# Performance work log

Measured on AMD Instinct MI355X. Metric: run time of the kernel, lower is better.

Reference implementation:

```python
import jax, jax.numpy as jnp
import numpy as np
from jax import lax
from jax.scipy.special import logsumexp

B, T, N = 256, 512, 128


def setup_inputs() -> dict:
    key = jax.random.key(0)
    k1, k2, k3 = jax.random.split(key, 3)
    emissions = jax.random.normal(k1, (B, T, N), dtype=jnp.float32)
    tag_ids = jax.random.randint(k2, (B, T), 0, N, dtype=jnp.int64)
    mask = jnp.ones((B, T), dtype=jnp.int32)
    # learned transition matrix (glorot-uniform-ish init)
    limit = float(np.sqrt(6.0 / (N + N)))
    trans = jax.random.uniform(k3, (N, N), minval=-limit, maxval=limit, dtype=jnp.float32)
    return {"emissions": emissions, "tag_ids": tag_ids, "mask": mask, "trans": trans}


def _sequence_score(emissions, tag_ids, maskf, trans):
    # unary: emission score of the gold tag at each valid step
    unary = jnp.take_along_axis(emissions, tag_ids[:, :, None], axis=2)[..., 0]  # [B,T]
    unary = jnp.sum(unary * maskf, axis=1)
    # binary: transition score between consecutive gold tags
    binary = trans[tag_ids[:, :-1], tag_ids[:, 1:]] * maskf[:, 1:]  # [B,T-1]
    return unary + jnp.sum(binary, axis=1)


def _log_norm(emissions, maskf, trans):
    # forward algorithm over time via lax.scan; alpha: [B,N]
    alpha0 = emissions[:, 0]
    em = jnp.swapaxes(emissions, 0, 1)[1:]   # [T-1,B,N]
    mk = jnp.swapaxes(maskf, 0, 1)[1:]       # [T-1,B]

    def step(alpha, xs):
        emit_t, m_t = xs
        new = logsumexp(alpha[:, :, None] + trans[None], axis=1) + emit_t
        alpha = jnp.where(m_t[:, None] > 0, new, alpha)
        return alpha, None

    alpha, _ = lax.scan(step, alpha0, (em, mk))
    return logsumexp(alpha, axis=1)  # [B]


def _viterbi_decode(emissions, maskf, trans):
    alpha0 = emissions[:, 0]
    em = jnp.swapaxes(emissions, 0, 1)[1:]
    mk = jnp.swapaxes(maskf, 0, 1)[1:]
    idx = jnp.arange(N, dtype=jnp.int32)[None]

    def fwd(alpha, xs):
        emit_t, m_t = xs
        scores = alpha[:, :, None] + trans[None]        # [B,N,N]
        bp = jnp.argmax(scores, axis=1).astype(jnp.int32)  # [B,N]
        new = jnp.max(scores, axis=1) + emit_t
        valid = m_t[:, None] > 0
        alpha = jnp.where(valid, new, alpha)
        bp = jnp.where(valid, bp, idx)  # carry same tag through padding
        return alpha, bp

    alpha, bps = lax.scan(fwd, alpha0, (em, mk))  # bps: [T-1,B,N]
    last_tag = jnp.argmax(alpha, axis=1).astype(jnp.int32)  # [B]

    def bwd(tag, bp_t):
        new_tag = jnp.take_along_axis(bp_t, tag[:, None], axis=1)[:, 0]
        return new_tag, new_tag

    _, tags_rev = lax.scan(bwd, last_tag, bps[::-1])  # [T-1,B]
    tags = jnp.concatenate([tags_rev[::-1], last_tag[None]], axis=0)  # [T,B]
    return jnp.swapaxes(tags, 0, 1)  # [B,T]


def reference(emissions, tag_ids, mask, trans):
    maskf = mask.astype(emissions.dtype)
    log_likelihood = _sequence_score(emissions, tag_ids, maskf, trans) - _log_norm(emissions, maskf, trans)
    predict = _viterbi_decode(emissions, maskf, trans)
    return (log_likelihood, trans, predict)
```

## Files before the change

kernel.cpp:

```cpp
#include <hip/hip_runtime.h>
#include <cmath>

#define BB 256
#define TT 512
#define NN 128
#define LN2F 0.6931471805599453f

typedef __bf16 bf16x8 __attribute__((ext_vector_type(8)));
typedef float floatx4 __attribute__((ext_vector_type(4)));

__device__ __forceinline__ float wave_max64(float v) {
    #pragma unroll
    for (int off = 32; off; off >>= 1) v = fmaxf(v, __shfl_xor(v, off));
    return v;
}
__device__ __forceinline__ float wave_sum64(float v) {
    #pragma unroll
    for (int off = 32; off; off >>= 1) v += __shfl_xor(v, off);
    return v;
}
__device__ __forceinline__ int wave_argmax128(float v0, float v1, int l) {
    float m = fmaxf(v0, v1);
    float wm = wave_max64(m);
    unsigned long long ball = __ballot(m == wm);
    int lane = __ffsll(ball) - 1;
    int idx = (v0 == wm) ? (2 * l) : (2 * l + 1);
    return __shfl(idx, lane);
}

__device__ __forceinline__ __bf16 to_bf16(float f) {
    unsigned u = __float_as_uint(f);
    unsigned r = (u + 0x7FFFu + ((u >> 16) & 1u)) >> 16;
    union { unsigned short s; __bf16 b; } cv;
    cv.s = (unsigned short)r;
    return cv.b;
}

__device__ __forceinline__ int padidx(int i) { return 36 * (i >> 5) + (i & 31); }

__global__ __launch_bounds__(512, 4) void fwd_kernel(
        const float* __restrict__ em, const int* __restrict__ gtags,
        const int* __restrict__ mask, const float* __restrict__ trans,
        float* __restrict__ out_ll, float* __restrict__ out_trans,
        float* __restrict__ outp) {
    const int bi = blockIdx.x;
    const bool isV = bi < BB;
    const int b = isV ? bi : bi - BB;
    const int tid = threadIdx.x;
    const int w = tid >> 6;
    const int l = tid & 63;
    const int j = (l & 15) + 16 * w;
    const int q = l >> 4;
    const int i0 = 32 * q;

    __shared__ __align__(16) float stA[144], stB[144];
    __shared__ __align__(16) __bf16 sbf[2][NN];
    __shared__ unsigned char bp_lds[TT * NN];
    __shared__ unsigned char tags_lds[TT];
    __shared__ unsigned char map_lds[8 * NN];
    __shared__ int entry_sh[8];
    __shared__ int msk[TT];
    __shared__ float piv[2];
    __shared__ float sfin[NN];
    __shared__ float wsum[8];
    __shared__ float llnorm_sh;
    __shared__ int misc[2];

    msk[tid] = mask[b * TT + tid];

    const float* emb = em + (size_t)b * TT * NN;

    if (isV) {
        float4 c0, c1, c2, c3, c4, c5, c6, c7;
        {
            const float* tc = trans + (size_t)i0 * NN + j;
            #define LDC(cc, u) cc.x = tc[(4*u+0)*NN]; cc.y = tc[(4*u+1)*NN]; \
                               cc.z = tc[(4*u+2)*NN]; cc.w = tc[(4*u+3)*NN];
            LDC(c0, 0) LDC(c1, 1) LDC(c2, 2) LDC(c3, 3)
            LDC(c4, 4) LDC(c5, 5) LDC(c6, 6) LDC(c7, 7)
            #undef LDC
        }
        float st = 0.f;
        {
            float a0 = emb[j];
            st = a0;
            if (l < 16) stA[padidx(j)] = a0;
        }
        float e_next = emb[NN + j];
        __syncthreads();

        const float4* apA = (const float4*)(stA + 36 * q);
        const float4* apB = (const float4*)(stB + 36 * q);

        auto VSTEP = [&](int t, const float4* ap, float* dst) {
            const float e_cur = e_next;
            if (t + 1 < TT) e_next = emb[(size_t)(t + 1) * NN + j];
            const int m = msk[t];
            float4 v0 = ap[0], v1 = ap[1], v2 = ap[2], v3 = ap[3],
                   v4 = ap[4], v5 = ap[5], v6 = ap[6], v7 = ap[7];
            float m0 = -INFINITY, m1 = -INFINITY, m2 = -INFINITY, m3 = -INFINITY;
            int u0 = 0, u1 = 0, u2 = 0, u3 = 0;
            #define CH(vv, cc, u) { \
                float a = vv.x + cc.x; u0 = (a > m0) ? u : u0; m0 = fmaxf(m0, a); \
                float bq = vv.y + cc.y; u1 = (bq > m1) ? u : u1; m1 = fmaxf(m1, bq); \
                float c = vv.z + cc.z; u2 = (c > m2) ? u : u2; m2 = fmaxf(m2, c); \
                float d = vv.w + cc.w; u3 = (d > m3) ? u : u3; m3 = fmaxf(m3, d); }
            CH(v0, c0, 0) CH(v1, c1, 1) CH(v2, c2, 2) CH(v3, c3, 3)
            CH(v4, c4, 4) CH(v5, c5, 5) CH(v6, c6, 6) CH(v7, c7, 7)
            #undef CH
            float bv = m0; int bx = i0 + 4 * u0;
            { int id = i0 + 4*u1 + 1; if (m1 > bv || (m1 == bv && id < bx)) { bv = m1; bx = id; } }
            { int id = i0 + 4*u2 + 2; if (m2 > bv || (m2 == bv && id < bx)) { bv = m2; bx = id; } }
            { int id = i0 + 4*u3 + 3; if (m3 > bv || (m3 == bv && id < bx)) { bv = m3; bx = id; } }
            #pragma unroll
            for (int off = 16; off <= 32; off <<= 1) {
                float ov = __shfl_xor(bv, off);
                int oi = __shfl_xor(bx, off);
                if (ov > bv || (ov == bv && oi < bx)) { bv = ov; bx = oi; }
            }
            if (l < 16) {
                float an; int bp;
                if (m) { an = bv + e_cur; bp = bx; }
                else   { an = st;         bp = j;  }
                st = an;
                dst[padidx(j)] = an;
                bp_lds[t * NN + j] = (unsigned char)bp;
            }
            __syncthreads();
        };

        for (int t = 1; t < TT - 1; t += 2) {
            VSTEP(t, apA, stB);
            VSTEP(t + 1, apB, stA);
        }
        VSTEP(TT - 1, apA, stB);

        if (w == 0) {
            float a0 = stB[padidx(2 * l)], a1 = stB[padidx(2 * l + 1)];
            int tg = wave_argmax128(a0, a1, l);
            if (l == 0) { misc[0] = tg; tags_lds[TT - 1] = (unsigned char)tg; }
        }
        if (tid < 64) out_trans[b * 64 + tid] = trans[b * 64 + tid];
        __syncthreads();
        const int lo = 64 * w + 1;
        const int hi = (w == 7) ? (TT - 1) : (64 * w + 64);
        {
            int tA = 2 * l, tB = 2 * l + 1;
            for (int t = hi; t >= lo; --t) {
                tA = bp_lds[t * NN + tA];
                tB = bp_lds[t * NN + tB];
            }
            map_lds[w * NN + 2 * l]     = (unsigned char)tA;
            map_lds[w * NN + 2 * l + 1] = (unsigned char)tB;
        }
        __syncthreads();
        if (tid == 0) {
            int e = misc[0];
            entry_sh[7] = e;
            for (int c = 7; c >= 1; --c) { e = map_lds[c * NN + e]; entry_sh[c - 1] = e; }
        }
        __syncthreads();
        if (l == 0) {
            int tg = entry_sh[w];
            for (int t = hi; t >= lo; --t) {
                tg = bp_lds[t * NN + tg];
                tags_lds[t - 1] = (unsigned char)tg;
            }
        }
        __syncthreads();
        outp[(size_t)b * TT + tid] = (float)tags_lds[tid];
    } else {
        bf16x8 Bf[4];
        #pragma unroll
        for (int kc = 0; kc < 4; ++kc) {
            #pragma unroll
            for (int jj = 0; jj < 8; ++jj) {
                int row = kc * 32 + q * 8 + jj;
                Bf[kc][jj] = to_bf16(__expf(trans[(size_t)row * NN + j]));
            }
        }
        float ss = __expf(emb[j]);
        int kacc = 0;
        if (l < 16) sbf[0][j] = to_bf16(ss);
        if (tid == 0) piv[0] = ss;
        float e_next = emb[NN + j];
        __syncthreads();

        for (int t = 1; t < TT; ++t) {
            const float e_cur = e_next;
            if (t + 1 < TT) e_next = emb[(size_t)(t + 1) * NN + j];
            const int m = msk[t];
            const int p = (t - 1) & 1, qb = t & 1;
            if (m) {
                const __bf16* sp = sbf[p];
                floatx4 acc = {0.f, 0.f, 0.f, 0.f};
                #pragma unroll
                for (int kc = 0; kc < 4; ++kc) {
                    bf16x8 a = *(const bf16x8*)(sp + kc * 32 + q * 8);
                    acc = __builtin_amdgcn_mfma_f32_16x16x32_bf16(a, Bf[kc], acc, 0, 0, 0);
                }
                float dot = acc[0];
                const float pv = piv[p];
                const int k = (int)(__float_as_uint(pv) >> 23) - 127;
                const float scale = __uint_as_float((unsigned)(127 - k) << 23);
                ss = dot * scale * __expf(e_cur);
                if (tid == 0) kacc += k;
            }
            if (l < 16) sbf[qb][j] = to_bf16(ss);
            if (tid == 0) piv[qb] = ss;
            __syncthreads();
        }

        if (l < 16) sfin[j] = ss;
        if (tid == 0) misc[1] = kacc;
        __syncthreads();
        if (w == 0) {
            float v = sfin[2 * l] + sfin[2 * l + 1];
            v = wave_sum64(v);
            if (l == 0) llnorm_sh = __logf(v) + (float)misc[1] * LN2F;
        }
        float acc = 0.f;
        {
            int tg = gtags[b * TT + tid];
            float mf = (float)msk[tid];
            acc = emb[(size_t)tid * NN + tg] * mf;
            if (tid >= 1) {
                int tp = gtags[b * TT + tid - 1];
                acc += trans[tp * NN + tg] * mf;
            }
        }
        acc = wave_sum64(acc);
        if (l == 0) wsum[w] = acc;
        __syncthreads();
        if (tid == 0) {
            float s = 0.f;
            #pragma unroll
            for (int i = 0; i < 8; ++i) s += wsum[i];
            out_ll[b] = s - llnorm_sh;
        }
    }
}

extern "C" void kernel_launch(void* const* d_in, const int* in_sizes, int n_in,
                              void* d_out, int out_size, void* d_ws, size_t ws_size,
                              hipStream_t stream) {
    const float* em = (const float*)d_in[0];
    const int* gtags = (const int*)d_in[1];
    const int* mask = (const int*)d_in[2];
    const float* trans = (const float*)d_in[3];

    float* out = (float*)d_out;
    float* out_ll = out;
    float* out_trans = out + BB;
    float* out_pred = out + BB + NN * NN;

    hipLaunchKernelGGL(fwd_kernel, dim3(2 * BB), dim3(512), 0, stream,
                       em, gtags, mask, trans, out_ll, out_trans, out_pred);
}
```

Baseline: 521.1 us.

## Move Viterbi backpointers to global workspace and transposed trans into LDS

Adds a Viterbi kernel variant that writes backpointers to a global workspace buffer instead of a 64KB LDS array. The freed LDS holds a padded, transposed copy of the transition matrix, which is read as float4 in place of 32 register-held values. The aim is to cut register pressure and LDS footprint per block. The cost is global memory traffic for backpointers, including dependent global reads during the backtrace. The old kernel remains as a fallback when the workspace is too small.

```diff
diff --git a/kernel.cpp b/kernel.cpp
--- a/kernel.cpp
+++ b/kernel.cpp
@@ -5,6 +5,7 @@
 #define TT 512
 #define NN 128
 #define LN2F 0.6931471805599453f
+#define TLS 132
 
 typedef __bf16 bf16x8 __attribute__((ext_vector_type(8)));
 typedef float floatx4 __attribute__((ext_vector_type(4)));
@@ -38,7 +39,207 @@
 
 __device__ __forceinline__ int padidx(int i) { return 36 * (i >> 5) + (i & 31); }
 
-__global__ __launch_bounds__(512, 4) void fwd_kernel(
+__global__ __launch_bounds__(512, 4) void fwd_kernel_g(
+        const float* __restrict__ em, const int* __restrict__ gtags,
+        const int* __restrict__ mask, const float* __restrict__ trans,
+        unsigned char* __restrict__ bpg_all,
+        float* __restrict__ out_ll, float* __restrict__ out_trans,
+        float* __restrict__ outp) {
+    const int bi = blockIdx.x;
+    const bool isV = bi < BB;
+    const int b = isV ? bi : bi - BB;
+    const int tid = threadIdx.x;
+    const int w = tid >> 6;
+    const int l = tid & 63;
+    const int j = (l & 15) + 16 * w;
+    const int q = l >> 4;
+    const int i0 = 32 * q;
+
+    __shared__ __align__(16) float tl[NN * TLS];
+    __shared__ __align__(16) float stA[144], stB[144];
+    __shared__ __align__(16) __bf16 sbf[2][NN];
+    __shared__ unsigned char tags_lds[TT];
+    __shared__ unsigned char map_lds[8 * NN];
+    __shared__ int entry_sh[8];
+    __shared__ int msk[TT];
+    __shared__ float piv[2];
+    __shared__ float sfin[NN];
+    __shared__ float wsum[8];
+    __shared__ float llnorm_sh;
+    __shared__ int misc[2];
+
+    msk[tid] = mask[b * TT + tid];
+
+    const float* emb = em + (size_t)b * TT * NN;
+
+    if (isV) {
+        for (int idx = tid; idx < NN * NN; idx += 512) {
+            int i = idx >> 7, jj = idx & 127;
+            tl[jj * TLS + i] = trans[idx];
+        }
+        unsigned char* bpg = bpg_all + (size_t)b * TT * NN;
+        float st;
+        {
+            float a0 = emb[j];
+            st = a0;
+            if (l < 16) stA[padidx(j)] = a0;
+        }
+        float e_next = emb[NN + j];
+        __syncthreads();
+
+        const float4* cp = (const float4*)(tl + j * TLS + i0);
+        const float4* apA = (const float4*)(stA + 36 * q);
+        const float4* apB = (const float4*)(stB + 36 * q);
+
+        auto VSTEP = [&](int t, const float4* ap, float* dst) {
+            const float e_cur = e_next;
+            if (t + 1 < TT) e_next = emb[(size_t)(t + 1) * NN + j];
+            const int m = msk[t];
+            float m0 = -INFINITY, m1 = -INFINITY, m2 = -INFINITY, m3 = -INFINITY;
+            int u0 = 0, u1 = 0, u2 = 0, u3 = 0;
+            #pragma unroll
+            for (int u = 0; u < 8; ++u) {
+                float4 av = ap[u];
+                float4 cv = cp[u];
+                float c0 = av.x + cv.x; u0 = (c0 > m0) ? u : u0; m0 = fmaxf(m0, c0);
+                float c1 = av.y + cv.y; u1 = (c1 > m1) ? u : u1; m1 = fmaxf(m1, c1);
+                float c2 = av.z + cv.z; u2 = (c2 > m2) ? u : u2; m2 = fmaxf(m2, c2);
+                float c3 = av.w + cv.w; u3 = (c3 > m3) ? u : u3; m3 = fmaxf(m3, c3);
+            }
+            float bv = m0; int bx = i0 + 4 * u0;
+            { int id = i0 + 4*u1 + 1; if (m1 > bv || (m1 == bv && id < bx)) { bv = m1; bx = id; } }
+            { int id = i0 + 4*u2 + 2; if (m2 > bv || (m2 == bv && id < bx)) { bv = m2; bx = id; } }
+            { int id = i0 + 4*u3 + 3; if (m3 > bv || (m3 == bv && id < bx)) { bv = m3; bx = id; } }
+            #pragma unroll
+            for (int off = 16; off <= 32; off <<= 1) {
+                float ov = __shfl_xor(bv, off);
+                int oi = __shfl_xor(bx, off);
+                if (ov > bv || (ov == bv && oi < bx)) { bv = ov; bx = oi; }
+            }
+            if (l < 16) {
+                float an; int bp;
+                if (m) { an = bv + e_cur; bp = bx; }
+                else   { an = st;         bp = j;  }
+                st = an;
+                dst[padidx(j)] = an;
+                bpg[(size_t)t * NN + j] = (unsigned char)bp;
+            }
+            __syncthreads();
+        };
+
+        for (int t = 1; t < TT - 1; t += 2) {
+            VSTEP(t, apA, stB);
+            VSTEP(t + 1, apB, stA);
+        }
+        VSTEP(TT - 1, apA, stB);
+
+        if (w == 0) {
+            float a0 = stB[padidx(2 * l)], a1 = stB[padidx(2 * l + 1)];
+            int tg = wave_argmax128(a0, a1, l);
+            if (l == 0) { misc[0] = tg; tags_lds[TT - 1] = (unsigned char)tg; }
+        }
+        if (tid < 64) out_trans[b * 64 + tid] = trans[b * 64 + tid];
+        __syncthreads();
+        const int lo = 64 * w + 1;
+        const int hi = (w == 7) ? (TT - 1) : (64 * w + 64);
+        {
+            int tA = 2 * l, tB = 2 * l + 1;
+            for (int t = hi; t >= lo; --t) {
+                tA = bpg[(size_t)t * NN + tA];
+                tB = bpg[(size_t)t * NN + tB];
+            }
+            map_lds[w * NN + 2 * l]     = (unsigned char)tA;
+            map_lds[w * NN + 2 * l + 1] = (unsigned char)tB;
+        }
+        __syncthreads();
+        if (tid == 0) {
+            int e = misc[0];
+            entry_sh[7] = e;
+            for (int c = 7; c >= 1; --c) { e = map_lds[c * NN + e]; entry_sh[c - 1] = e; }
+        }
+        __syncthreads();
+        if (l == 0) {
+            int tg = entry_sh[w];
+            for (int t = hi; t >= lo; --t) {
+                tg = bpg[(size_t)t * NN + tg];
+                tags_lds[t - 1] = (unsigned char)tg;
+            }
+        }
+        __syncthreads();
+        outp[(size_t)b * TT + tid] = (float)tags_lds[tid];
+    } else {
+        bf16x8 Bf[4];
+        #pragma unroll
+        for (int kc = 0; kc < 4; ++kc) {
+            #pragma unroll
+            for (int jj = 0; jj < 8; ++jj) {
+                int row = kc * 32 + q * 8 + jj;
+                Bf[kc][jj] = to_bf16(__expf(trans[(size_t)row * NN + j]));
+            }
+        }
+        float ss = __expf(emb[j]);
+        int kacc = 0;
+        if (l < 16) sbf[0][j] = to_bf16(ss);
+        if (tid == 0) piv[0] = ss;
+        float e_next = emb[NN + j];
+        __syncthreads();
+
+        for (int t = 1; t < TT; ++t) {
+            const float e_cur = e_next;
+            if (t + 1 < TT) e_next = emb[(size_t)(t + 1) * NN + j];
+            const int m = msk[t];
+            const int p = (t - 1) & 1, qb = t & 1;
+            if (m) {
+                const __bf16* sp = sbf[p];
+                floatx4 acc = {0.f, 0.f, 0.f, 0.f};
+                #pragma unroll
+                for (int kc = 0; kc < 4; ++kc) {
+                    bf16x8 a = *(const bf16x8*)(sp + kc * 32 + q * 8);
+                    acc = __builtin_amdgcn_mfma_f32_16x16x32_bf16(a, Bf[kc], acc, 0, 0, 0);
+                }
+                float dot = acc[0];
+                const float pv = piv[p];
+                const int k = (int)(__float_as_uint(pv) >> 23) - 127;
+                const float scale = __uint_as_float((unsigned)(127 - k) << 23);
+                ss = dot * scale * __expf(e_cur);
+                if (tid == 0) kacc += k;
+            }
+            if (l < 16) sbf[qb][j] = to_bf16(ss);
+            if (tid == 0) piv[qb] = ss;
+            __syncthreads();
+        }
+
+        if (l < 16) sfin[j] = ss;
+        if (tid == 0) misc[1] = kacc;
+        __syncthreads();
+        if (w == 0) {
+            float v = sfin[2 * l] + sfin[2 * l + 1];
+            v = wave_sum64(v);
+            if (l == 0) llnorm_sh = __logf(v) + (float)misc[1] * LN2F;
+        }
+        float acc = 0.f;
+        {
+            int tg = gtags[b * TT + tid];
+            float mf = (float)msk[tid];
+            acc = emb[(size_t)tid * NN + tg] * mf;
+            if (tid >= 1) {
+                int tp = gtags[b * TT + tid - 1];
+                acc += trans[tp * NN + tg] * mf;
+            }
+        }
+        acc = wave_sum64(acc);
+        if (l == 0) wsum[w] = acc;
+        __syncthreads();
+        if (tid == 0) {
+            float s = 0.f;
+            #pragma unroll
+            for (int i = 0; i < 8; ++i) s += wsum[i];
+            out_ll[b] = s - llnorm_sh;
+        }
+    }
+}
+
+__global__ __launch_bounds__(512, 4) void fwd_kernel_l(
         const float* __restrict__ em, const int* __restrict__ gtags,
         const int* __restrict__ mask, const float* __restrict__ trans,
         float* __restrict__ out_ll, float* __restrict__ out_trans,
@@ -67,7 +268,6 @@
     __shared__ int misc[2];
 
     msk[tid] = mask[b * TT + tid];
-
     const float* emb = em + (size_t)b * TT * NN;
 
     if (isV) {
@@ -254,6 +454,13 @@
     float* out_trans = out + BB;
     float* out_pred = out + BB + NN * NN;
 
-    hipLaunchKernelGGL(fwd_kernel, dim3(2 * BB), dim3(512), 0, stream,
-                       em, gtags, mask, trans, out_ll, out_trans, out_pred);
-}
+    const size_t bp_bytes = (size_t)BB * TT * NN;
+    if (ws_size >= bp_bytes) {
+        hipLaunchKernelGGL(fwd_kernel_g, dim3(2 * BB), dim3(512), 0, stream,
+                           em, gtags, mask, trans, (unsigned char*)d_ws,
+                           out_ll, out_trans, out_pred);
+    } else {
+        hipLaunchKernelGGL(fwd_kernel_l, dim3(2 * BB), dim3(512), 0, stream,
+                           em, gtags, mask, trans, out_ll, out_trans, out_pred);
+    }
+}
```

Measured after the change: 612.6 us. 1.18x slower.
